# Kernel optimization log

Measured on AMD Instinct MI355X. Metric: run time of the kernel, lower is better.

## Reference

```python
import jax, jax.numpy as jnp
import numpy as np

W = 128; H = 128; NEAR = 0.1; FAR = 10.0; EPS = 1e-8
B = 1; V = 512; F = 1024


def _perspective(cf, cc):
    # OpenGL-convention projection, returned transposed for row-vector multiply
    f = 0.5 * (cf[0] + cf[1]); pco = 0.5
    right = (W - (cc[0] + pco)) * (NEAR / f)
    left = -(cc[0] + pco) * (NEAR / f)
    top = (cc[1] + pco) * (NEAR / f)
    bottom = -(H - cc[1] + pco) * (NEAR / f)
    z = jnp.zeros(())
    m = jnp.stack([
        jnp.stack([2.0 * NEAR / (right - left), z, (right + left) / (right - left), z]),
        jnp.stack([z, 2.0 * NEAR / (top - bottom), (top + bottom) / (top - bottom), z]),
        jnp.stack([z, z, jnp.full((), -(FAR + NEAR) / (FAR - NEAR)), jnp.full((), -2.0 * FAR * NEAR / (FAR - NEAR))]),
        jnp.stack([z, z, jnp.full((), -1.0), z]),
    ])
    return m.T


def _rodrigues(r):
    theta = jnp.sqrt(jnp.sum(r * r) + 1e-12)
    k = r / theta
    zz = jnp.zeros(())
    K = jnp.stack([
        jnp.stack([zz, -k[2], k[1]]),
        jnp.stack([k[2], zz, -k[0]]),
        jnp.stack([-k[1], k[0], zz]),
    ])
    return jnp.eye(3) + jnp.sin(theta) * K + (1.0 - jnp.cos(theta)) * (K @ K)


def _view_matrix(rt, t):
    # row-vector convention: v' = v @ M, M = rodrigues^T composed with translation-in-last-row
    R = _rodrigues(rt)
    Mr = jnp.eye(4).at[:3, :3].set(R.T)
    Mt = jnp.eye(4).at[3, :3].set(t)
    return Mr @ Mt


def _rasterize_one(vs_xy, z_ndc, inv_w, valid_tri, f, vc, bgcolor, px, py):
    # vs_xy [V,2] screen coords, z_ndc [V], inv_w [V]; f [F,3] int; pixels px,py [P]
    a = vs_xy[f[:, 0]]; b = vs_xy[f[:, 1]]; c = vs_xy[f[:, 2]]  # [F,2]
    x = px[:, None]; y = py[:, None]  # [P,1]
    def E(p, q):  # signed edge function, broadcast to [P,F]
        return (q[:, 0] - p[:, 0]) * (y - p[:, 1]) - (q[:, 1] - p[:, 1]) * (x - p[:, 0])
    w0 = E(b, c); w1 = E(c, a); w2 = E(a, b)  # [P,F]
    area = (b[:, 0] - a[:, 0]) * (c[:, 1] - a[:, 1]) - (b[:, 1] - a[:, 1]) * (c[:, 0] - a[:, 0])  # [F]
    area_safe = jnp.where(jnp.abs(area) > EPS, area, 1.0)
    b0 = w0 / area_safe; b1 = w1 / area_safe; b2 = w2 / area_safe
    za = z_ndc[f[:, 0]]; zb = z_ndc[f[:, 1]]; zc = z_ndc[f[:, 2]]
    z = b0 * za + b1 * zb + b2 * zc  # [P,F] interpolated NDC depth
    inside = ((b0 >= 0) & (b1 >= 0) & (b2 >= 0) & (jnp.abs(area) > EPS)
              & valid_tri[None, :] & (z >= -1.0) & (z <= 1.0))
    depth = jnp.where(inside, z, jnp.inf)
    best = jnp.argmin(depth, axis=1)  # [P] z-buffer winner
    covered = jnp.take_along_axis(depth, best[:, None], 1)[:, 0] <= 1.0
    take = lambda m: jnp.take_along_axis(m, best[:, None], 1)[:, 0]
    bs = jnp.stack([take(b0), take(b1), take(b2)], -1)  # [P,3]
    tri = f[best]          # [P,3]
    iw = inv_w[tri]        # [P,3]
    col = vc[tri]          # [P,3,C]
    den = jnp.sum(bs * iw, -1)
    den = jnp.where(jnp.abs(den) > EPS, den, 1.0)
    color = jnp.einsum('pk,pk,pkc->pc', bs, iw, col) / den[:, None]  # perspective-correct
    return jnp.where(covered[:, None], color, bgcolor[None, :])  # [P,C]


def reference(v, vc, f, bgcolor, camera_f, camera_c, camera_t, camera_rt):
    view = _view_matrix(camera_rt, camera_t)
    proj = _perspective(camera_f, camera_c)
    vh = jnp.concatenate([v, jnp.ones_like(v[..., :1])], -1)  # [B,V,4]
    clip = vh @ (view @ proj)                                 # [B,V,4]
    wc = clip[..., 3]
    valid_v = wc > EPS                                        # in front of camera
    w_safe = jnp.where(valid_v, wc, 1.0)
    ndc = clip[..., :3] / w_safe[..., None]
    xs = (ndc[..., 0] * 0.5 + 0.5) * W
    ys = (0.5 - ndc[..., 1] * 0.5) * H
    vs_xy = jnp.stack([xs, ys], -1)                           # [B,V,2]
    inv_w = 1.0 / w_safe
    valid_tri = valid_v[:, f].all(-1)                         # [B,F]
    gy, gx = jnp.meshgrid(jnp.arange(H, dtype=jnp.float32) + 0.5,
                          jnp.arange(W, dtype=jnp.float32) + 0.5, indexing='ij')
    px = gx.reshape(-1); py = gy.reshape(-1)
    img = jax.vmap(lambda xy, zn, iw, vt: _rasterize_one(xy, zn, iw, vt, f, vc, bgcolor, px, py))(
        vs_xy, ndc[..., 2], inv_w, valid_tri)
    return img.reshape(v.shape[0], H, W, vc.shape[-1])


def setup_inputs() -> dict:
    key = jax.random.key(0)
    k1, k2, k3 = jax.random.split(key, 3)
    u = jax.random.uniform(k1, (B, V, 3), dtype=jnp.float32)
    # x,y in [-0.8,0.8], z in [-3,-1] (camera looks along -z)
    vtx = jnp.stack([u[..., 0] * 1.6 - 0.8, u[..., 1] * 1.6 - 0.8, -(1.0 + 2.0 * u[..., 2])], -1)
    vc = jax.random.uniform(k2, (V, 3), dtype=jnp.float32)
    f = jax.random.randint(k3, (F, 3), 0, V, dtype=jnp.int32)
    return {
        'v': vtx,
        'vc': vc,
        'f': f,
        'bgcolor': jnp.zeros((3,), jnp.float32),
        'camera_f': jnp.array([128.0, 128.0], jnp.float32),
        'camera_c': jnp.array([64.0, 64.0], jnp.float32),
        'camera_t': jnp.zeros((3,), jnp.float32),
        'camera_rt': jnp.zeros((3,), jnp.float32),
    }
```

## Files before the change

### kernel.cpp

```cpp
#include <hip/hip_runtime.h>
#include <math.h>
#include <stdint.h>

#define NV 512
#define NF 1024
#define TRI_STRIDE 16
#define NGROUP 16
#define CHUNK 64


__global__ __launch_bounds__(1024) void setup_kernel(
    const float* __restrict__ v, const int* __restrict__ fidx,
    const float* __restrict__ camf, const float* __restrict__ camc,
    const float* __restrict__ camt, const float* __restrict__ camrt,
    double* __restrict__ vdata, double* __restrict__ tridata,
    double2* __restrict__ afT, unsigned long long* __restrict__ keys)
{
#pragma clang fp contract(off)
  __shared__ double sM[16];
  __shared__ double sxs[NV], sys_[NV], szn[NV];
  __shared__ int svld[NV];
  const int tid = threadIdx.x;

  for (int i = tid; i < 16384; i += 1024) keys[i] = ~0ull;

  if (tid == 0) {
    float r0f = camrt[0], r1f = camrt[1], r2f = camrt[2];
    float th = sqrtf(((r0f * r0f + r1f * r1f) + r2f * r2f) + 1e-12f);
    float k0 = r0f / th, k1 = r1f / th, k2 = r2f / th;
    float sthf = sinf(th);
    float cthf = 1.0f - cosf(th);
    double K[3][3] = {{0.0, -(double)k2, (double)k1},
                      {(double)k2, 0.0, -(double)k0},
                      {-(double)k1, (double)k0, 0.0}};
    double KK[3][3];
    for (int i = 0; i < 3; ++i)
      for (int j = 0; j < 3; ++j)
        KK[i][j] = (K[i][0] * K[0][j] + K[i][1] * K[1][j]) + K[i][2] * K[2][j];
    double R[3][3];
    for (int i = 0; i < 3; ++i)
      for (int j = 0; j < 3; ++j) {
        double e = (i == j) ? 1.0 : 0.0;
        R[i][j] = (e + (double)sthf * K[i][j]) + (double)cthf * KK[i][j];
      }
    double Mr[4][4], Mt[4][4];
    for (int i = 0; i < 4; ++i)
      for (int j = 0; j < 4; ++j) {
        Mr[i][j] = (i == j) ? 1.0 : 0.0;
        Mt[i][j] = (i == j) ? 1.0 : 0.0;
      }
    for (int i = 0; i < 3; ++i)
      for (int j = 0; j < 3; ++j) Mr[i][j] = R[j][i];
    Mt[3][0] = (double)camt[0]; Mt[3][1] = (double)camt[1]; Mt[3][2] = (double)camt[2];
    double view[4][4];
    for (int i = 0; i < 4; ++i)
      for (int j = 0; j < 4; ++j)
        view[i][j] = ((Mr[i][0] * Mt[0][j] + Mr[i][1] * Mt[1][j]) +
                      Mr[i][2] * Mt[2][j]) + Mr[i][3] * Mt[3][j];
    float fcam = 0.5f * (camf[0] + camf[1]);
    float nf = 0.1f / fcam;
    float ccx = camc[0], ccy = camc[1];
    float right = (128.0f - (ccx + 0.5f)) * nf;
    float left = -(ccx + 0.5f) * nf;
    float top = (ccy + 0.5f) * nf;
    float bottom = -((128.0f - ccy) + 0.5f) * nf;
    float m00f = 0.2f / (right - left);
    float m02f = (right + left) / (right - left);
    float m11f = 0.2f / (top - bottom);
    float m12f = (top + bottom) / (top - bottom);
    double P[4][4] = {
        {(double)m00f, 0.0, (double)m02f, 0.0},
        {0.0, (double)m11f, (double)m12f, 0.0},
        {0.0, 0.0, -(10.0 + 0.1) / (10.0 - 0.1),
         -2.0 * 10.0 * 0.1 / (10.0 - 0.1)},
        {0.0, 0.0, -1.0, 0.0}};
    for (int i = 0; i < 4; ++i)
      for (int j = 0; j < 4; ++j)
        sM[i * 4 + j] = ((view[i][0] * P[j][0] + view[i][1] * P[j][1]) +
                         view[i][2] * P[j][2]) + view[i][3] * P[j][3];
  }
  __syncthreads();

  if (tid < NV) {
    double x = (double)v[tid * 3 + 0];
    double y = (double)v[tid * 3 + 1];
    double zz = (double)v[tid * 3 + 2];
    double c0 = ((x * sM[0] + y * sM[4]) + zz * sM[8]) + sM[12];
    double c1 = ((x * sM[1] + y * sM[5]) + zz * sM[9]) + sM[13];
    double c2 = ((x * sM[2] + y * sM[6]) + zz * sM[10]) + sM[14];
    double c3 = ((x * sM[3] + y * sM[7]) + zz * sM[11]) + sM[15];
    int valid = c3 > 1e-8;
    double wsafe = valid ? c3 : 1.0;
    double n0 = c0 / wsafe, n1 = c1 / wsafe, n2 = c2 / wsafe;
    double xs = (n0 * 0.5 + 0.5) * 128.0;
    double ys = (0.5 - n1 * 0.5) * 128.0;
    double iw = 1.0 / wsafe;
    sxs[tid] = xs; sys_[tid] = ys; szn[tid] = n2; svld[tid] = valid;
    vdata[0 * NV + tid] = xs;
    vdata[1 * NV + tid] = ys;
    vdata[2 * NV + tid] = n2;
    vdata[3 * NV + tid] = iw;
  }
  __syncthreads();

  {
    int i0 = fidx[tid * 3 + 0], i1 = fidx[tid * 3 + 1], i2 = fidx[tid * 3 + 2];
    double ax = sxs[i0], ay = sys_[i0];
    double bx = sxs[i1], by = sys_[i1];
    double cx = sxs[i2], cy = sys_[i2];
    double p1 = (bx - ax) * (cy - ay);
    double p2 = (by - ay) * (cx - ax);
    double area = p1 - p2;
    bool ok = (fabs(area) > 1e-8) && svld[i0] && svld[i1] && svld[i2];
    double s = (area > 0.0) ? 1.0 : -1.0;
    double inv_abs = ok ? s / area : 1.0;
    double kk0 = szn[i0] * inv_abs, kk1 = szn[i1] * inv_abs, kk2 = szn[i2] * inv_abs;

    double* td = tridata + tid * TRI_STRIDE;
    td[0] = bx;  td[1] = by;  td[2] = cx;  td[3] = cy;  td[4] = ax;  td[5] = ay;
    td[6] = s * (cx - bx);  td[7] = s * (cy - by);
    td[8] = s * (ax - cx);  td[9] = s * (ay - cy);
    td[10] = s * (bx - ax); td[11] = s * (by - ay);
    td[12] = kk0; td[13] = kk1; td[14] = kk2;
    td[15] = inv_abs;

    double e0x = cx - bx, e0y = cy - by;
    double e1x = ax - cx, e1y = ay - cy;
    double e2x = bx - ax, e2y = by - ay;
    double A0 = -s * e0y, B0 = s * e0x, C0 = s * (e0y * bx - e0x * by);
    double A1 = -s * e1y, B1 = s * e1x, C1 = s * (e1y * cx - e1x * cy);
    double A2 = -s * e2y, B2 = s * e2x, C2 = s * (e2y * ax - e2x * ay);
    double Az = (A0 * kk0 + A1 * kk1) + A2 * kk2;
    double Bz = (B0 * kk0 + B1 * kk1) + B2 * kk2;
    double Cz = (C0 * kk0 + C1 * kk1) + C2 * kk2;
    double absarea = ok ? (s * area) : __builtin_nan("");
    afT[0 * NF + tid] = make_double2(A0, B0);
    afT[1 * NF + tid] = make_double2(C0, A1);
    afT[2 * NF + tid] = make_double2(B1, C1);
    afT[3 * NF + tid] = make_double2(Az, Bz);
    afT[4 * NF + tid] = make_double2(Cz, absarea);
  }
}

__global__ __launch_bounds__(256) void raster_kernel(
    const double2* __restrict__ afT, unsigned long long* __restrict__ keys)
{
  __shared__ double2 sc[5][CHUNK];
  const int tid = threadIdx.x;
  const int tile = blockIdx.x;
  const int group = blockIdx.y;
  const int tbase = group * CHUNK;

  for (int i = tid; i < 5 * CHUNK; i += 256) {
    int f = i >> 6, t = i & 63;
    sc[f][t] = afT[f * NF + tbase + t];
  }
  __syncthreads();

  const int x = ((tile & 7) << 4) + (tid & 15);
  const int y = ((tile >> 3) << 4) + (tid >> 4);
  const double px = (double)x + 0.5, py = (double)y + 0.5;

  double bestz = INFINITY;
  int besti = -1;
#pragma unroll 4
  for (int t = 0; t < CHUNK; ++t) {
    double2 c0 = sc[0][t];
    double2 c1 = sc[1][t];
    double2 c2 = sc[2][t];
    double2 c3 = sc[3][t];
    double2 c4 = sc[4][t];
    double w0 = (c0.x * px + c0.y * py) + c1.x;
    double w1 = (c1.y * px + c2.x * py) + c2.y;
    double z  = (c3.x * px + c3.y * py) + c4.x;
    double w2 = (c4.y - w0) - w1;
    bool ins = (w0 >= 0.0) & (w1 >= 0.0) & (w2 >= 0.0) &
               (z >= -1.0) & (z <= 1.0) & (z < bestz);
    bestz = ins ? z : bestz;
    besti = ins ? (tbase + t) : besti;
  }
  if (besti >= 0) {
    unsigned long long zq = (unsigned long long)((bestz + 1.0) * 4503599627370496.0);
    atomicMin(&keys[y * 128 + x], (zq << 10) | (unsigned long long)besti);
  }
}

__global__ __launch_bounds__(256) void color_kernel(
    const unsigned long long* __restrict__ keys,
    const double* __restrict__ vdata, const double* __restrict__ tridata,
    const int* __restrict__ fidx, const float* __restrict__ vc,
    const float* __restrict__ bg, float* __restrict__ out)
{
  const int p = blockIdx.x * 256 + threadIdx.x;
  if (p >= 16384) return;
  const int x = p & 127, y = p >> 7;
  unsigned long long key = keys[p];
  float cr, cg, cb;
  if (key == ~0ull) {
    cr = bg[0]; cg = bg[1]; cb = bg[2];
  } else {
    unsigned int t = (unsigned int)(key & 1023ull);
    const double* td = tridata + t * TRI_STRIDE;
    double px = (double)x + 0.5, py = (double)y + 0.5;
    double w0 = td[6] * (py - td[1]) - td[7] * (px - td[0]);
    double w1 = td[8] * (py - td[3]) - td[9] * (px - td[2]);
    double w2 = td[10] * (py - td[5]) - td[11] * (px - td[4]);
    double inv = td[15];
    double b0 = w0 * inv, b1 = w1 * inv, b2 = w2 * inv;
    int i0 = fidx[t * 3 + 0], i1 = fidx[t * 3 + 1], i2 = fidx[t * 3 + 2];
    double t0 = b0 * vdata[3 * NV + i0];
    double t1 = b1 * vdata[3 * NV + i1];
    double t2 = b2 * vdata[3 * NV + i2];
    double den = (t0 + t1) + t2;
    if (!(fabs(den) > 1e-8)) den = 1.0;
    cr = (float)((((t0 * (double)vc[i0 * 3 + 0] + t1 * (double)vc[i1 * 3 + 0]) +
                   t2 * (double)vc[i2 * 3 + 0])) / den);
    cg = (float)((((t0 * (double)vc[i0 * 3 + 1] + t1 * (double)vc[i1 * 3 + 1]) +
                   t2 * (double)vc[i2 * 3 + 1])) / den);
    cb = (float)((((t0 * (double)vc[i0 * 3 + 2] + t1 * (double)vc[i1 * 3 + 2]) +
                   t2 * (double)vc[i2 * 3 + 2])) / den);
  }
  out[p * 3 + 0] = cr;
  out[p * 3 + 1] = cg;
  out[p * 3 + 2] = cb;
}

extern "C" void kernel_launch(void* const* d_in, const int* in_sizes, int n_in,
                              void* d_out, int out_size, void* d_ws, size_t ws_size,
                              hipStream_t stream) {
  const float* v = (const float*)d_in[0];
  const float* vc = (const float*)d_in[1];
  const int* fidx = (const int*)d_in[2];
  const float* bg = (const float*)d_in[3];
  const float* camf = (const float*)d_in[4];
  const float* camc = (const float*)d_in[5];
  const float* camt = (const float*)d_in[6];
  const float* camrt = (const float*)d_in[7];
  float* out = (float*)d_out;

  char* ws = (char*)d_ws;
  unsigned long long* keys = (unsigned long long*)ws;
  double* vdata = (double*)(ws + 131072);
  double* tridata = (double*)(ws + 147456);
  double2* afT = (double2*)(ws + 278528);

  setup_kernel<<<1, 1024, 0, stream>>>(v, fidx, camf, camc, camt, camrt,
                                       vdata, tridata, afT, keys);
  raster_kernel<<<dim3(64, NGROUP), 256, 0, stream>>>(afT, keys);
  color_kernel<<<64, 256, 0, stream>>>(keys, vdata, tridata, fidx, vc, bg, out);
}
```

Baseline: 93.05 us.

## Fuse setup into raster kernel with redundant per-block vertex and triangle setup

Removes the single-block setup kernel and has every raster block recompute the camera matrix, the projection of all 512 vertices, and the edge coefficients for its own 64-triangle chunk directly into shared memory. Designated blocks write vdata and tridata for the color pass. Key initialization moves to hipMemsetAsync. This drops a serial one-block launch and the global round-trip of the coefficient buffer, at the cost of redundant vertex work in all 1024 blocks and an extra memset operation.

```diff
diff --git a/kernel.cpp b/kernel.cpp
--- a/kernel.cpp
+++ b/kernel.cpp
@@ -9,151 +9,145 @@
 #define CHUNK 64
 
 
-__global__ __launch_bounds__(1024) void setup_kernel(
+__global__ __launch_bounds__(256, 4) void render_kernel(
     const float* __restrict__ v, const int* __restrict__ fidx,
     const float* __restrict__ camf, const float* __restrict__ camc,
     const float* __restrict__ camt, const float* __restrict__ camrt,
     double* __restrict__ vdata, double* __restrict__ tridata,
-    double2* __restrict__ afT, unsigned long long* __restrict__ keys)
+    unsigned long long* __restrict__ keys)
 {
-#pragma clang fp contract(off)
   __shared__ double sM[16];
   __shared__ double sxs[NV], sys_[NV], szn[NV];
   __shared__ int svld[NV];
-  const int tid = threadIdx.x;
-
-  for (int i = tid; i < 16384; i += 1024) keys[i] = ~0ull;
-
-  if (tid == 0) {
-    float r0f = camrt[0], r1f = camrt[1], r2f = camrt[2];
-    float th = sqrtf(((r0f * r0f + r1f * r1f) + r2f * r2f) + 1e-12f);
-    float k0 = r0f / th, k1 = r1f / th, k2 = r2f / th;
-    float sthf = sinf(th);
-    float cthf = 1.0f - cosf(th);
-    double K[3][3] = {{0.0, -(double)k2, (double)k1},
-                      {(double)k2, 0.0, -(double)k0},
-                      {-(double)k1, (double)k0, 0.0}};
-    double KK[3][3];
-    for (int i = 0; i < 3; ++i)
-      for (int j = 0; j < 3; ++j)
-        KK[i][j] = (K[i][0] * K[0][j] + K[i][1] * K[1][j]) + K[i][2] * K[2][j];
-    double R[3][3];
-    for (int i = 0; i < 3; ++i)
-      for (int j = 0; j < 3; ++j) {
-        double e = (i == j) ? 1.0 : 0.0;
-        R[i][j] = (e + (double)sthf * K[i][j]) + (double)cthf * KK[i][j];
-      }
-    double Mr[4][4], Mt[4][4];
-    for (int i = 0; i < 4; ++i)
-      for (int j = 0; j < 4; ++j) {
-        Mr[i][j] = (i == j) ? 1.0 : 0.0;
-        Mt[i][j] = (i == j) ? 1.0 : 0.0;
-      }
-    for (int i = 0; i < 3; ++i)
-      for (int j = 0; j < 3; ++j) Mr[i][j] = R[j][i];
-    Mt[3][0] = (double)camt[0]; Mt[3][1] = (double)camt[1]; Mt[3][2] = (double)camt[2];
-    double view[4][4];
-    for (int i = 0; i < 4; ++i)
-      for (int j = 0; j < 4; ++j)
-        view[i][j] = ((Mr[i][0] * Mt[0][j] + Mr[i][1] * Mt[1][j]) +
-                      Mr[i][2] * Mt[2][j]) + Mr[i][3] * Mt[3][j];
-    float fcam = 0.5f * (camf[0] + camf[1]);
-    float nf = 0.1f / fcam;
-    float ccx = camc[0], ccy = camc[1];
-    float right = (128.0f - (ccx + 0.5f)) * nf;
-    float left = -(ccx + 0.5f) * nf;
-    float top = (ccy + 0.5f) * nf;
-    float bottom = -((128.0f - ccy) + 0.5f) * nf;
-    float m00f = 0.2f / (right - left);
-    float m02f = (right + left) / (right - left);
-    float m11f = 0.2f / (top - bottom);
-    float m12f = (top + bottom) / (top - bottom);
-    double P[4][4] = {
-        {(double)m00f, 0.0, (double)m02f, 0.0},
-        {0.0, (double)m11f, (double)m12f, 0.0},
-        {0.0, 0.0, -(10.0 + 0.1) / (10.0 - 0.1),
-         -2.0 * 10.0 * 0.1 / (10.0 - 0.1)},
-        {0.0, 0.0, -1.0, 0.0}};
-    for (int i = 0; i < 4; ++i)
-      for (int j = 0; j < 4; ++j)
-        sM[i * 4 + j] = ((view[i][0] * P[j][0] + view[i][1] * P[j][1]) +
-                         view[i][2] * P[j][2]) + view[i][3] * P[j][3];
-  }
-  __syncthreads();
-
-  if (tid < NV) {
-    double x = (double)v[tid * 3 + 0];
-    double y = (double)v[tid * 3 + 1];
-    double zz = (double)v[tid * 3 + 2];
-    double c0 = ((x * sM[0] + y * sM[4]) + zz * sM[8]) + sM[12];
-    double c1 = ((x * sM[1] + y * sM[5]) + zz * sM[9]) + sM[13];
-    double c2 = ((x * sM[2] + y * sM[6]) + zz * sM[10]) + sM[14];
-    double c3 = ((x * sM[3] + y * sM[7]) + zz * sM[11]) + sM[15];
-    int valid = c3 > 1e-8;
-    double wsafe = valid ? c3 : 1.0;
-    double n0 = c0 / wsafe, n1 = c1 / wsafe, n2 = c2 / wsafe;
-    double xs = (n0 * 0.5 + 0.5) * 128.0;
-    double ys = (0.5 - n1 * 0.5) * 128.0;
-    double iw = 1.0 / wsafe;
-    sxs[tid] = xs; sys_[tid] = ys; szn[tid] = n2; svld[tid] = valid;
-    vdata[0 * NV + tid] = xs;
-    vdata[1 * NV + tid] = ys;
-    vdata[2 * NV + tid] = n2;
-    vdata[3 * NV + tid] = iw;
-  }
-  __syncthreads();
-
-  {
-    int i0 = fidx[tid * 3 + 0], i1 = fidx[tid * 3 + 1], i2 = fidx[tid * 3 + 2];
-    double ax = sxs[i0], ay = sys_[i0];
-    double bx = sxs[i1], by = sys_[i1];
-    double cx = sxs[i2], cy = sys_[i2];
-    double p1 = (bx - ax) * (cy - ay);
-    double p2 = (by - ay) * (cx - ax);
-    double area = p1 - p2;
-    bool ok = (fabs(area) > 1e-8) && svld[i0] && svld[i1] && svld[i2];
-    double s = (area > 0.0) ? 1.0 : -1.0;
-    double inv_abs = ok ? s / area : 1.0;
-    double kk0 = szn[i0] * inv_abs, kk1 = szn[i1] * inv_abs, kk2 = szn[i2] * inv_abs;
-
-    double* td = tridata + tid * TRI_STRIDE;
-    td[0] = bx;  td[1] = by;  td[2] = cx;  td[3] = cy;  td[4] = ax;  td[5] = ay;
-    td[6] = s * (cx - bx);  td[7] = s * (cy - by);
-    td[8] = s * (ax - cx);  td[9] = s * (ay - cy);
-    td[10] = s * (bx - ax); td[11] = s * (by - ay);
-    td[12] = kk0; td[13] = kk1; td[14] = kk2;
-    td[15] = inv_abs;
-
-    double e0x = cx - bx, e0y = cy - by;
-    double e1x = ax - cx, e1y = ay - cy;
-    double e2x = bx - ax, e2y = by - ay;
-    double A0 = -s * e0y, B0 = s * e0x, C0 = s * (e0y * bx - e0x * by);
-    double A1 = -s * e1y, B1 = s * e1x, C1 = s * (e1y * cx - e1x * cy);
-    double A2 = -s * e2y, B2 = s * e2x, C2 = s * (e2y * ax - e2x * ay);
-    double Az = (A0 * kk0 + A1 * kk1) + A2 * kk2;
-    double Bz = (B0 * kk0 + B1 * kk1) + B2 * kk2;
-    double Cz = (C0 * kk0 + C1 * kk1) + C2 * kk2;
-    double absarea = ok ? (s * area) : __builtin_nan("");
-    afT[0 * NF + tid] = make_double2(A0, B0);
-    afT[1 * NF + tid] = make_double2(C0, A1);
-    afT[2 * NF + tid] = make_double2(B1, C1);
-    afT[3 * NF + tid] = make_double2(Az, Bz);
-    afT[4 * NF + tid] = make_double2(Cz, absarea);
-  }
-}
-
-__global__ __launch_bounds__(256) void raster_kernel(
-    const double2* __restrict__ afT, unsigned long long* __restrict__ keys)
-{
   __shared__ double2 sc[5][CHUNK];
   const int tid = threadIdx.x;
   const int tile = blockIdx.x;
   const int group = blockIdx.y;
   const int tbase = group * CHUNK;
 
-  for (int i = tid; i < 5 * CHUNK; i += 256) {
-    int f = i >> 6, t = i & 63;
-    sc[f][t] = afT[f * NF + tbase + t];
+  {
+#pragma clang fp contract(off)
+    if (tid == 0) {
+      float r0f = camrt[0], r1f = camrt[1], r2f = camrt[2];
+      float th = sqrtf(((r0f * r0f + r1f * r1f) + r2f * r2f) + 1e-12f);
+      float k0 = r0f / th, k1 = r1f / th, k2 = r2f / th;
+      float sthf = sinf(th);
+      float cthf = 1.0f - cosf(th);
+      double K[3][3] = {{0.0, -(double)k2, (double)k1},
+                        {(double)k2, 0.0, -(double)k0},
+                        {-(double)k1, (double)k0, 0.0}};
+      double KK[3][3];
+      for (int i = 0; i < 3; ++i)
+        for (int j = 0; j < 3; ++j)
+          KK[i][j] = (K[i][0] * K[0][j] + K[i][1] * K[1][j]) + K[i][2] * K[2][j];
+      double R[3][3];
+      for (int i = 0; i < 3; ++i)
+        for (int j = 0; j < 3; ++j) {
+          double e = (i == j) ? 1.0 : 0.0;
+          R[i][j] = (e + (double)sthf * K[i][j]) + (double)cthf * KK[i][j];
+        }
+      double Mr[4][4], Mt[4][4];
+      for (int i = 0; i < 4; ++i)
+        for (int j = 0; j < 4; ++j) {
+          Mr[i][j] = (i == j) ? 1.0 : 0.0;
+          Mt[i][j] = (i == j) ? 1.0 : 0.0;
+        }
+      for (int i = 0; i < 3; ++i)
+        for (int j = 0; j < 3; ++j) Mr[i][j] = R[j][i];
+      Mt[3][0] = (double)camt[0]; Mt[3][1] = (double)camt[1]; Mt[3][2] = (double)camt[2];
+      double view[4][4];
+      for (int i = 0; i < 4; ++i)
+        for (int j = 0; j < 4; ++j)
+          view[i][j] = ((Mr[i][0] * Mt[0][j] + Mr[i][1] * Mt[1][j]) +
+                        Mr[i][2] * Mt[2][j]) + Mr[i][3] * Mt[3][j];
+      float fcam = 0.5f * (camf[0] + camf[1]);
+      float nf = 0.1f / fcam;
+      float ccx = camc[0], ccy = camc[1];
+      float right = (128.0f - (ccx + 0.5f)) * nf;
+      float left = -(ccx + 0.5f) * nf;
+      float top = (ccy + 0.5f) * nf;
+      float bottom = -((128.0f - ccy) + 0.5f) * nf;
+      float m00f = 0.2f / (right - left);
+      float m02f = (right + left) / (right - left);
+      float m11f = 0.2f / (top - bottom);
+      float m12f = (top + bottom) / (top - bottom);
+      double P[4][4] = {
+          {(double)m00f, 0.0, (double)m02f, 0.0},
+          {0.0, (double)m11f, (double)m12f, 0.0},
+          {0.0, 0.0, -(10.0 + 0.1) / (10.0 - 0.1),
+           -2.0 * 10.0 * 0.1 / (10.0 - 0.1)},
+          {0.0, 0.0, -1.0, 0.0}};
+      for (int i = 0; i < 4; ++i)
+        for (int j = 0; j < 4; ++j)
+          sM[i * 4 + j] = ((view[i][0] * P[j][0] + view[i][1] * P[j][1]) +
+                           view[i][2] * P[j][2]) + view[i][3] * P[j][3];
+    }
+    __syncthreads();
+
+    for (int i = tid; i < NV; i += 256) {
+      double x = (double)v[i * 3 + 0];
+      double y = (double)v[i * 3 + 1];
+      double zz = (double)v[i * 3 + 2];
+      double c0 = ((x * sM[0] + y * sM[4]) + zz * sM[8]) + sM[12];
+      double c1 = ((x * sM[1] + y * sM[5]) + zz * sM[9]) + sM[13];
+      double c2 = ((x * sM[2] + y * sM[6]) + zz * sM[10]) + sM[14];
+      double c3 = ((x * sM[3] + y * sM[7]) + zz * sM[11]) + sM[15];
+      int valid = c3 > 1e-8;
+      double wsafe = valid ? c3 : 1.0;
+      double n0 = c0 / wsafe, n1 = c1 / wsafe, n2 = c2 / wsafe;
+      double xs = (n0 * 0.5 + 0.5) * 128.0;
+      double ys = (0.5 - n1 * 0.5) * 128.0;
+      double iw = 1.0 / wsafe;
+      sxs[i] = xs; sys_[i] = ys; szn[i] = n2; svld[i] = valid;
+      if (tile == 0 && group == 0) {
+        vdata[0 * NV + i] = xs;
+        vdata[1 * NV + i] = ys;
+        vdata[2 * NV + i] = n2;
+        vdata[3 * NV + i] = iw;
+      }
+    }
+    __syncthreads();
+
+    if (tid < CHUNK) {
+      const int t = tbase + tid;
+      int i0 = fidx[t * 3 + 0], i1 = fidx[t * 3 + 1], i2 = fidx[t * 3 + 2];
+      double ax = sxs[i0], ay = sys_[i0];
+      double bx = sxs[i1], by = sys_[i1];
+      double cx = sxs[i2], cy = sys_[i2];
+      double p1 = (bx - ax) * (cy - ay);
+      double p2 = (by - ay) * (cx - ax);
+      double area = p1 - p2;
+      bool ok = (fabs(area) > 1e-8) && svld[i0] && svld[i1] && svld[i2];
+      double s = (area > 0.0) ? 1.0 : -1.0;
+      double inv_abs = ok ? s / area : 1.0;
+      double kk0 = szn[i0] * inv_abs, kk1 = szn[i1] * inv_abs, kk2 = szn[i2] * inv_abs;
+
+      if (tile == 0) {
+        double* td = tridata + t * TRI_STRIDE;
+        td[0] = bx;  td[1] = by;  td[2] = cx;  td[3] = cy;  td[4] = ax;  td[5] = ay;
+        td[6] = s * (cx - bx);  td[7] = s * (cy - by);
+        td[8] = s * (ax - cx);  td[9] = s * (ay - cy);
+        td[10] = s * (bx - ax); td[11] = s * (by - ay);
+        td[12] = kk0; td[13] = kk1; td[14] = kk2;
+        td[15] = inv_abs;
+      }
+
+      double e0x = cx - bx, e0y = cy - by;
+      double e1x = ax - cx, e1y = ay - cy;
+      double e2x = bx - ax, e2y = by - ay;
+      double A0 = -s * e0y, B0 = s * e0x, C0 = s * (e0y * bx - e0x * by);
+      double A1 = -s * e1y, B1 = s * e1x, C1 = s * (e1y * cx - e1x * cy);
+      double A2 = -s * e2y, B2 = s * e2x, C2 = s * (e2y * ax - e2x * ay);
+      double Az = (A0 * kk0 + A1 * kk1) + A2 * kk2;
+      double Bz = (B0 * kk0 + B1 * kk1) + B2 * kk2;
+      double Cz = (C0 * kk0 + C1 * kk1) + C2 * kk2;
+      double absarea = ok ? (s * area) : __builtin_nan("");
+      sc[0][tid] = make_double2(A0, B0);
+      sc[1][tid] = make_double2(C0, A1);
+      sc[2][tid] = make_double2(B1, C1);
+      sc[3][tid] = make_double2(Az, Bz);
+      sc[4][tid] = make_double2(Cz, absarea);
+    }
   }
   __syncthreads();
 
@@ -242,10 +236,9 @@
   unsigned long long* keys = (unsigned long long*)ws;
   double* vdata = (double*)(ws + 131072);
   double* tridata = (double*)(ws + 147456);
-  double2* afT = (double2*)(ws + 278528);
-
-  setup_kernel<<<1, 1024, 0, stream>>>(v, fidx, camf, camc, camt, camrt,
-                                       vdata, tridata, afT, keys);
-  raster_kernel<<<dim3(64, NGROUP), 256, 0, stream>>>(afT, keys);
+
+  hipMemsetAsync(keys, 0xFF, 16384 * sizeof(unsigned long long), stream);
+  render_kernel<<<dim3(64, NGROUP), 256, 0, stream>>>(
+      v, fidx, camf, camc, camt, camrt, vdata, tridata, keys);
   color_kernel<<<64, 256, 0, stream>>>(keys, vdata, tridata, fidx, vc, bg, out);
 }
```

New measurement: 89.69 us. -3.6%, faster.
